# Optimization experiments

Measured on AMD Instinct MI355X. Metric: run time of the kernel, lower is better.

## Reference

```python
import jax, jax.numpy as jnp
import numpy as np


def setup_inputs() -> dict:
    key = jax.random.key(0)
    k_x, k_q, k_k, k_v = jax.random.split(key, 4)
    B, S, F, U = 8, 2048, 1024, 256
    x = jax.random.normal(k_x, (B, S, F), dtype=jnp.float32)
    Wq = jax.random.normal(k_q, (F, U), dtype=jnp.float32) * 0.05
    Wk = jax.random.normal(k_k, (F, U), dtype=jnp.float32) * 0.05
    Wv = jax.random.normal(k_v, (F, U), dtype=jnp.float32) * 0.05
    return {"x": x, "Wq": Wq, "Wk": Wk, "Wv": Wv}


def reference(x, Wq, Wk, Wv):
    # x: [B, S, F]; projections tanh-activated: [B, S, U]
    xQ = jnp.tanh(jnp.einsum("bsf,fu->bsu", x, Wq))
    xK = jnp.tanh(jnp.einsum("bsf,fu->bsu", x, Wk))
    xV = jnp.tanh(jnp.einsum("bsf,fu->bsu", x, Wv))
    scale = 1.0 / jnp.sqrt(jnp.asarray(x.shape[-1], dtype=jnp.float32))
    scores = jnp.einsum("bsu,btu->bst", xQ, xK) * scale  # [B, S, S]
    weights = jax.nn.softmax(scores, axis=-1)
    out = jnp.einsum("bst,btu->bsu", weights, xV)  # return_sequences=True
    return out
```

## Files before the change

kernel.cpp:

```cpp
#include <hip/hip_runtime.h>
#include <math.h>

#define B_ 8
#define S_ 2048
#define F_ 1024
#define U_ 256
#define M_ (B_ * S_)

typedef __attribute__((ext_vector_type(8))) short bf16x8;
typedef __attribute__((ext_vector_type(4))) float f32x4;
typedef __attribute__((ext_vector_type(16))) float f32x16;
typedef unsigned short ushort_t;

__device__ __forceinline__ unsigned short f2bf(float x) {
    unsigned u = __builtin_bit_cast(unsigned, x);
    unsigned r = (u + 0x7fffu + ((u >> 16) & 1u)) >> 16;
    return (unsigned short)r;
}
__device__ __forceinline__ float bf2f(unsigned short b) {
    return __builtin_bit_cast(float, ((unsigned)b) << 16);
}
__device__ __forceinline__ void gload16(const void* g, void* l) {
    __builtin_amdgcn_global_load_lds(
        (const __attribute__((address_space(1))) unsigned int*)g,
        (__attribute__((address_space(3))) unsigned int*)l, 16, 0, 0);
}
__device__ __forceinline__ f32x4 zero4() {
    f32x4 v; v[0] = 0.f; v[1] = 0.f; v[2] = 0.f; v[3] = 0.f; return v;
}

__global__ __launch_bounds__(256) void convw_kernel(
    const float* __restrict__ Wq, const float* __restrict__ Wk,
    const float* __restrict__ Wv, ushort_t* __restrict__ Wp)
{
    const int ks   = blockIdx.x;
    const int wsel = blockIdx.y;
    const float* __restrict__ W = (wsel == 0) ? Wq : (wsel == 1) ? Wk : Wv;
    const int n = threadIdx.x;

    bf16x8 hv, lv;
    #pragma unroll
    for (int j = 0; j < 8; ++j) {
        float v = W[(size_t)(ks * 8 + j) * U_ + n];
        ushort_t h = f2bf(v);
        hv[j] = (short)h;
        lv[j] = (short)f2bf(v - bf2f(h));
    }
    size_t base = (size_t)wsel * 524288;
    *reinterpret_cast<bf16x8*>(&Wp[base + ((size_t)ks) * 2048 + n * 8]) = hv;
    *reinterpret_cast<bf16x8*>(&Wp[base + ((size_t)(128 + ks)) * 2048 + n * 8]) = lv;
}

__global__ __launch_bounds__(256, 2) void proj_mfma_kernel(
    const float* __restrict__ x,
    const ushort_t* __restrict__ Wp,
    ushort_t* __restrict__ qh_g, ushort_t* __restrict__ kh_g,
    ushort_t* __restrict__ vth_g)
{
    __shared__ float    As[2][128 * 16];
    __shared__ ushort_t Bs[2][2 * 2 * 256 * 8];

    const int orig = blockIdx.x;
    const int xcd  = orig & 7;
    const int idx  = orig >> 3;
    const int q3   = idx / 3;
    const int wsel = idx - q3 * 3;
    const int rt   = xcd * 16 + q3;
    const int row0 = rt * 128;

    const int tid = threadIdx.x;
    const int l = tid & 63, w = tid >> 6;
    const int m = l & 31, hi = l >> 5;

    const ushort_t* __restrict__ WpB = Wp + (size_t)wsel * 524288;

    f32x16 acc[4][2];
    #pragma unroll
    for (int mr = 0; mr < 4; ++mr)
        #pragma unroll
        for (int nf = 0; nf < 2; ++nf)
            #pragma unroll
            for (int r = 0; r < 16; ++r) acc[mr][nf][r] = 0.f;

    auto stageA = [&](int buf, int ks) {
        #pragma unroll
        for (int i = 0; i < 2; ++i) {
            int c = i * 256 + tid;
            int r = c >> 2, cc = c & 3;
            int cs = cc ^ ((r + (r >> 2)) & 3);
            const float* src = x + (size_t)(row0 + r) * F_ + ks * 16 + cs * 4;
            gload16(src, (char*)&As[buf][0] + (size_t)(i * 256 + w * 64) * 16);
        }
    };
    auto stageB = [&](int buf, int ks) {
        #pragma unroll
        for (int i = 0; i < 4; ++i) {
            int c = i * 256 + tid;
            int half = c >> 9, rem = c & 511;
            size_t so = (size_t)half * 262144 + (size_t)ks * 4096 + rem * 8;
            gload16(WpB + so, (char*)&Bs[buf][0] + (size_t)(i * 256 + w * 64) * 16);
        }
    };

    stageA(0, 0);
    stageB(0, 0);
    __syncthreads();

    for (int ks = 0; ks < 64; ++ks) {
        const int cur = ks & 1;
        if (ks < 63) { stageA(cur ^ 1, ks + 1); stageB(cur ^ 1, ks + 1); }

        const float*    Ac = &As[cur][0];
        const ushort_t* Bc = &Bs[cur][0];

        bf16x8 ah[4];
        #pragma unroll
        for (int mr = 0; mr < 4; ++mr) {
            const int r   = mr * 32 + m;
            const int swz = (r + (r >> 2)) & 3;
            const float4 a0 = *reinterpret_cast<const float4*>(
                &Ac[(size_t)(r * 4 + ((2 * hi) ^ swz)) * 4]);
            const float4 a1 = *reinterpret_cast<const float4*>(
                &Ac[(size_t)(r * 4 + ((2 * hi + 1) ^ swz)) * 4]);
            const float af[8] = {a0.x, a0.y, a0.z, a0.w, a1.x, a1.y, a1.z, a1.w};
            #pragma unroll
            for (int j = 0; j < 8; ++j) ah[mr][j] = (short)f2bf(af[j]);
        }
        #pragma unroll
        for (int nf = 0; nf < 2; ++nf) {
            const int nn = w * 64 + nf * 32 + m;
            const bf16x8 bh = *reinterpret_cast<const bf16x8*>(
                &Bc[(size_t)(hi * 2048 + nn * 8)]);
            const bf16x8 bl = *reinterpret_cast<const bf16x8*>(
                &Bc[(size_t)(4096 + hi * 2048 + nn * 8)]);
            #pragma unroll
            for (int mr = 0; mr < 4; ++mr) {
                acc[mr][nf] = __builtin_amdgcn_mfma_f32_32x32x16_bf16(ah[mr], bh, acc[mr][nf], 0, 0, 0);
                acc[mr][nf] = __builtin_amdgcn_mfma_f32_32x32x16_bf16(ah[mr], bl, acc[mr][nf], 0, 0, 0);
            }
        }
        __syncthreads();
    }

    #pragma unroll
    for (int mr = 0; mr < 4; ++mr) {
        const int row_base = row0 + mr * 32;
        if (wsel < 2) {
            ushort_t* __restrict__ hp = (wsel == 0) ? qh_g : kh_g;
            #pragma unroll
            for (int nf = 0; nf < 2; ++nf) {
                const int u = w * 64 + nf * 32 + m;
                #pragma unroll
                for (int reg = 0; reg < 16; ++reg) {
                    const int rl = (reg & 3) + 8 * (reg >> 2) + 4 * hi;
                    hp[(size_t)(row_base + rl) * U_ + u] =
                        f2bf(tanhf(acc[mr][nf][reg]));
                }
            }
        } else {
            const int b     = row0 >> 11;
            const int s_blk = (row0 & 2047) + mr * 32;
            #pragma unroll
            for (int nf = 0; nf < 2; ++nf) {
                const int u = w * 64 + nf * 32 + m;
                #pragma unroll
                for (int rg = 0; rg < 4; ++rg) {
                    ushort4 hv;
                    hv.x = f2bf(tanhf(acc[mr][nf][rg * 4 + 0]));
                    hv.y = f2bf(tanhf(acc[mr][nf][rg * 4 + 1]));
                    hv.z = f2bf(tanhf(acc[mr][nf][rg * 4 + 2]));
                    hv.w = f2bf(tanhf(acc[mr][nf][rg * 4 + 3]));
                    size_t off = ((size_t)b * U_ + u) * S_ + s_blk + 8 * rg + 4 * hi;
                    *reinterpret_cast<ushort4*>(&vth_g[off]) = hv;
                }
            }
        }
    }
}

__global__ __launch_bounds__(256, 2) void attn_mfma_kernel(
    const ushort_t* __restrict__ qh_g,
    const ushort_t* __restrict__ kh_g,
    const ushort_t* __restrict__ vth_g,
    float* __restrict__ O0, float* __restrict__ O1,
    float* __restrict__ ml)
{
    __shared__ ushort_t Kbuf[2][32 * 256];
    __shared__ ushort_t Vbuf[2][256 * 40];
    __shared__ ushort_t Pbuf[4][512];

    const int tid = threadIdx.x;
    const int l  = tid & 63, w = tid >> 6;
    const int kq = l & 15,  g = l >> 4;

    const int logical = (blockIdx.x & 7) * 64 + (blockIdx.x >> 3);
    const int b     = logical >> 6;
    const int qb    = (logical >> 1) & 31;
    const int khalf = logical & 1;
    const int qrow0 = b * S_ + qb * 64 + w * 16;
    const int kb0   = khalf * 1024;

    bf16x8 qh[8];
    {
        const ushort_t* qbh = qh_g + (size_t)(qrow0 + kq) * U_;
        #pragma unroll
        for (int us = 0; us < 8; ++us)
            qh[us] = *reinterpret_cast<const bf16x8*>(qbh + us * 32 + g * 8);
    }

    f32x4 O[16];
    #pragma unroll
    for (int nt = 0; nt < 16; ++nt) O[nt] = zero4();
    float m_run = -INFINITY, l_run = 0.f;

    auto stage = [&](int buf, int k0) {
        #pragma unroll
        for (int i = 0; i < 4; ++i) {
            int c = w * 256 + i * 64 + l;
            int key = c >> 5, uc = c & 31;
            int ucs = uc ^ (key & 7);
            size_t so = (size_t)(b * S_ + k0 + key) * U_ + ucs * 8;
            gload16(kh_g + so, &Kbuf[buf][(w * 256 + i * 64) * 8]);
        }
        #pragma unroll
        for (int i = 0; i < 5; ++i) {
            int c = w * 320 + i * 64 + l;
            int u = (c * 52429) >> 18;
            int kc = c - u * 5;
            size_t so = ((size_t)b * U_ + u) * S_ + k0 + kc * 8;
            const ushort_t* sh = (kc < 4) ? (vth_g + so) : vth_g;
            gload16(sh, &Vbuf[buf][(w * 320 + i * 64) * 8]);
        }
    };

    stage(0, kb0);
    asm volatile("s_waitcnt vmcnt(0)" ::: "memory");
    __builtin_amdgcn_s_barrier();

    const float scale = 0.03125f;

    for (int t = 0; t < 32; ++t) {
        const int cur = t & 1;
        if (t < 31) stage(cur ^ 1, kb0 + (t + 1) * 32);

        const ushort_t* Kh = Kbuf[cur];
        const ushort_t* Vh = Vbuf[cur];

        f32x4 hh0 = zero4(), hh1 = zero4();
        #pragma unroll
        for (int us = 0; us < 8; ++us) {
            int off0 = kq * 256 + ((us * 32 + g * 8) ^ ((kq & 7) * 8));
            bf16x8 k0h = *reinterpret_cast<const bf16x8*>(Kh + off0);
            hh0 = __builtin_amdgcn_mfma_f32_16x16x32_bf16(k0h, qh[us], hh0, 0, 0, 0);
            int off1 = off0 + 16 * 256;
            bf16x8 k1h = *reinterpret_cast<const bf16x8*>(Kh + off1);
            hh1 = __builtin_amdgcn_mfma_f32_16x16x32_bf16(k1h, qh[us], hh1, 0, 0, 0);
        }
        f32x4 s0 = hh0 * scale;
        f32x4 s1 = hh1 * scale;

        float tm = fmaxf(fmaxf(fmaxf(s0[0], s0[1]), fmaxf(s0[2], s0[3])),
                         fmaxf(fmaxf(s1[0], s1[1]), fmaxf(s1[2], s1[3])));
        tm = fmaxf(tm, __shfl_xor(tm, 16));
        tm = fmaxf(tm, __shfl_xor(tm, 32));
        float mn = fmaxf(m_run, tm);
        ushort_t ph0[4], ph1[4];
        float su = 0.f;
        #pragma unroll
        for (int r = 0; r < 4; ++r) {
            ph0[r] = f2bf(expf(s0[r] - mn)); su += bf2f(ph0[r]);
        }
        #pragma unroll
        for (int r = 0; r < 4; ++r) {
            ph1[r] = f2bf(expf(s1[r] - mn)); su += bf2f(ph1[r]);
        }
        su += __shfl_xor(su, 16);
        su += __shfl_xor(su, 32);
        float f = expf(m_run - mn);
        l_run = l_run * f + su;
        m_run = mn;

        {
            ushort4 a, c;
            a.x = ph0[0]; a.y = ph0[1]; a.z = ph0[2]; a.w = ph0[3];
            c.x = ph1[0]; c.y = ph1[1]; c.z = ph1[2]; c.w = ph1[3];
            int pw0 = ((g >> 1)) * 128 + kq * 8 + (g & 1) * 4;
            int pw1 = (2 + (g >> 1)) * 128 + kq * 8 + (g & 1) * 4;
            *reinterpret_cast<ushort4*>(&Pbuf[w][pw0]) = a;
            *reinterpret_cast<ushort4*>(&Pbuf[w][pw1]) = c;
        }

        float fr0 = __shfl(f, g * 4 + 0), fr1 = __shfl(f, g * 4 + 1);
        float fr2 = __shfl(f, g * 4 + 2), fr3 = __shfl(f, g * 4 + 3);
        #pragma unroll
        for (int nt = 0; nt < 16; ++nt) {
            O[nt][0] *= fr0; O[nt][1] *= fr1; O[nt][2] *= fr2; O[nt][3] *= fr3;
        }

        bf16x8 pa_h = *reinterpret_cast<const bf16x8*>(&Pbuf[w][g * 128 + kq * 8]);
        #pragma unroll
        for (int nt = 0; nt < 16; ++nt) {
            int vo = (nt * 16 + kq) * 40 + g * 8;
            bf16x8 vh = *reinterpret_cast<const bf16x8*>(Vh + vo);
            O[nt] = __builtin_amdgcn_mfma_f32_16x16x32_bf16(pa_h, vh, O[nt], 0, 0, 0);
        }

        asm volatile("s_waitcnt vmcnt(0)" ::: "memory");
        __builtin_amdgcn_s_barrier();
    }

    float* __restrict__ Op = khalf ? O1 : O0;
    #pragma unroll
    for (int nt = 0; nt < 16; ++nt) {
        const int col = nt * 16 + kq;
        Op[(size_t)(qrow0 + g * 4 + 0) * U_ + col] = O[nt][0];
        Op[(size_t)(qrow0 + g * 4 + 1) * U_ + col] = O[nt][1];
        Op[(size_t)(qrow0 + g * 4 + 2) * U_ + col] = O[nt][2];
        Op[(size_t)(qrow0 + g * 4 + 3) * U_ + col] = O[nt][3];
    }
    if (g == 0) {
        ml[((size_t)khalf * M_ + qrow0 + kq) * 2 + 0] = m_run;
        ml[((size_t)khalf * M_ + qrow0 + kq) * 2 + 1] = l_run;
    }
}

__global__ __launch_bounds__(256) void merge_kernel(
    const float* __restrict__ O1, const float* __restrict__ ml,
    float* __restrict__ out)
{
    const int tid = threadIdx.x;
    const int row = blockIdx.x * 4 + (tid >> 6);
    const int c   = (tid & 63) * 4;

    const float m0 = ml[(size_t)row * 2 + 0];
    const float l0 = ml[(size_t)row * 2 + 1];
    const float m1 = ml[((size_t)M_ + row) * 2 + 0];
    const float l1 = ml[((size_t)M_ + row) * 2 + 1];
    const float Mx = fmaxf(m0, m1);
    float a0 = expf(m0 - Mx), a1 = expf(m1 - Mx);
    const float inv = 1.f / (a0 * l0 + a1 * l1);
    a0 *= inv; a1 *= inv;

    const size_t off = (size_t)row * U_ + c;
    const float4 o0 = *reinterpret_cast<const float4*>(out + off);
    const float4 o1 = *reinterpret_cast<const float4*>(O1 + off);
    float4 r;
    r.x = o0.x * a0 + o1.x * a1;
    r.y = o0.y * a0 + o1.y * a1;
    r.z = o0.z * a0 + o1.z * a1;
    r.w = o0.w * a0 + o1.w * a1;
    *reinterpret_cast<float4*>(out + off) = r;
}

extern "C" void kernel_launch(void* const* d_in, const int* in_sizes, int n_in,
                              void* d_out, int out_size, void* d_ws, size_t ws_size,
                              hipStream_t stream)
{
    (void)in_sizes; (void)n_in; (void)out_size; (void)ws_size;
    const float* x  = (const float*)d_in[0];
    const float* Wq = (const float*)d_in[1];
    const float* Wk = (const float*)d_in[2];
    const float* Wv = (const float*)d_in[3];
    float* out = (float*)d_out;

    ushort_t* ws = (ushort_t*)d_ws;
    const size_t T = (size_t)M_ * U_;
    ushort_t* qh_g  = ws;
    ushort_t* kh_g  = ws + T;
    ushort_t* vth_g = ws + 2 * T;
    ushort_t* Wp    = ws + 3 * T;
    float*    O1    = (float*)(ws + 3 * T + 1572864);
    float*    ml    = O1 + T;

    convw_kernel<<<dim3(128, 3), 256, 0, stream>>>(Wq, Wk, Wv, Wp);

    proj_mfma_kernel<<<dim3(384), 256, 0, stream>>>(
        x, Wp, qh_g, kh_g, vth_g);

    attn_mfma_kernel<<<dim3(512), 256, 0, stream>>>(
        qh_g, kh_g, vth_g, out, O1, ml);

    merge_kernel<<<dim3(M_ / 4), 256, 0, stream>>>(O1, ml, out);
}
```

Baseline: 181.8 us.

## Pre-convert x to bf16 and stage bf16 tiles in projection GEMM

Adds a pass that converts x to bf16 once into workspace. The projection kernel then loads bf16 tiles directly, with no per-iteration fp32-to-bf16 conversion in the inner loop. This halves the bytes each of the three weight-select blocks reads for x. The K step doubles to 32, so there are half as many iterations and barriers, and the LDS layout is simplified. The cost is an extra kernel launch plus a write and read of a 32MB bf16 copy. That copy aliases the O1 region, which relies on the workspace being large enough.

```diff
diff --git a/kernel.cpp b/kernel.cpp
--- a/kernel.cpp
+++ b/kernel.cpp
@@ -29,6 +29,23 @@
     f32x4 v; v[0] = 0.f; v[1] = 0.f; v[2] = 0.f; v[3] = 0.f; return v;
 }
 
+__global__ __launch_bounds__(256) void convx_kernel(
+    const float* __restrict__ x, ushort_t* __restrict__ xb)
+{
+    const size_t base = ((size_t)blockIdx.x * 256 + threadIdx.x) * 16;
+    #pragma unroll
+    for (int i = 0; i < 2; ++i) {
+        const float4 v0 = *reinterpret_cast<const float4*>(x + base + i * 8);
+        const float4 v1 = *reinterpret_cast<const float4*>(x + base + i * 8 + 4);
+        bf16x8 o;
+        o[0] = (short)f2bf(v0.x); o[1] = (short)f2bf(v0.y);
+        o[2] = (short)f2bf(v0.z); o[3] = (short)f2bf(v0.w);
+        o[4] = (short)f2bf(v1.x); o[5] = (short)f2bf(v1.y);
+        o[6] = (short)f2bf(v1.z); o[7] = (short)f2bf(v1.w);
+        *reinterpret_cast<bf16x8*>(xb + base + i * 8) = o;
+    }
+}
+
 __global__ __launch_bounds__(256) void convw_kernel(
     const float* __restrict__ Wq, const float* __restrict__ Wk,
     const float* __restrict__ Wv, ushort_t* __restrict__ Wp)
@@ -52,21 +69,20 @@
 }
 
 __global__ __launch_bounds__(256, 2) void proj_mfma_kernel(
-    const float* __restrict__ x,
+    const ushort_t* __restrict__ xb,
     const ushort_t* __restrict__ Wp,
     ushort_t* __restrict__ qh_g, ushort_t* __restrict__ kh_g,
     ushort_t* __restrict__ vth_g)
 {
-    __shared__ float    As[2][128 * 16];
-    __shared__ ushort_t Bs[2][2 * 2 * 256 * 8];
+    __shared__ ushort_t As[2][4 * 128 * 8];
+    __shared__ ushort_t Bs[2][2 * 4 * 256 * 8];
 
     const int orig = blockIdx.x;
     const int xcd  = orig & 7;
     const int idx  = orig >> 3;
     const int q3   = idx / 3;
     const int wsel = idx - q3 * 3;
-    const int rt   = xcd * 16 + q3;
-    const int row0 = rt * 128;
+    const int row0 = (xcd * 16 + q3) * 128;
 
     const int tid = threadIdx.x;
     const int l = tid & 63, w = tid >> 6;
@@ -85,20 +101,20 @@
     auto stageA = [&](int buf, int ks) {
         #pragma unroll
         for (int i = 0; i < 2; ++i) {
-            int c = i * 256 + tid;
-            int r = c >> 2, cc = c & 3;
-            int cs = cc ^ ((r + (r >> 2)) & 3);
-            const float* src = x + (size_t)(row0 + r) * F_ + ks * 16 + cs * 4;
+            int ci = i * 256 + tid;
+            int c = ci >> 7, r = ci & 127;
+            const ushort_t* src = xb + (size_t)(row0 + r) * F_ + ks * 32 + c * 8;
             gload16(src, (char*)&As[buf][0] + (size_t)(i * 256 + w * 64) * 16);
         }
     };
     auto stageB = [&](int buf, int ks) {
         #pragma unroll
-        for (int i = 0; i < 4; ++i) {
-            int c = i * 256 + tid;
-            int half = c >> 9, rem = c & 511;
-            size_t so = (size_t)half * 262144 + (size_t)ks * 4096 + rem * 8;
-            gload16(WpB + so, (char*)&Bs[buf][0] + (size_t)(i * 256 + w * 64) * 16);
+        for (int i = 0; i < 8; ++i) {
+            int ci = i * 256 + tid;
+            int half = ci >> 10, rem = ci & 1023;
+            const ushort_t* src = WpB + (size_t)half * 262144
+                                  + (size_t)ks * 8192 + rem * 8;
+            gload16(src, (char*)&Bs[buf][0] + (size_t)(i * 256 + w * 64) * 16);
         }
     };
 
@@ -106,37 +122,33 @@
     stageB(0, 0);
     __syncthreads();
 
-    for (int ks = 0; ks < 64; ++ks) {
+    for (int ks = 0; ks < 32; ++ks) {
         const int cur = ks & 1;
-        if (ks < 63) { stageA(cur ^ 1, ks + 1); stageB(cur ^ 1, ks + 1); }
-
-        const float*    Ac = &As[cur][0];
+        if (ks < 31) { stageA(cur ^ 1, ks + 1); stageB(cur ^ 1, ks + 1); }
+
+        const ushort_t* Ac = &As[cur][0];
         const ushort_t* Bc = &Bs[cur][0];
 
-        bf16x8 ah[4];
-        #pragma unroll
-        for (int mr = 0; mr < 4; ++mr) {
-            const int r   = mr * 32 + m;
-            const int swz = (r + (r >> 2)) & 3;
-            const float4 a0 = *reinterpret_cast<const float4*>(
-                &Ac[(size_t)(r * 4 + ((2 * hi) ^ swz)) * 4]);
-            const float4 a1 = *reinterpret_cast<const float4*>(
-                &Ac[(size_t)(r * 4 + ((2 * hi + 1) ^ swz)) * 4]);
-            const float af[8] = {a0.x, a0.y, a0.z, a0.w, a1.x, a1.y, a1.z, a1.w};
-            #pragma unroll
-            for (int j = 0; j < 8; ++j) ah[mr][j] = (short)f2bf(af[j]);
-        }
-        #pragma unroll
-        for (int nf = 0; nf < 2; ++nf) {
-            const int nn = w * 64 + nf * 32 + m;
-            const bf16x8 bh = *reinterpret_cast<const bf16x8*>(
-                &Bc[(size_t)(hi * 2048 + nn * 8)]);
-            const bf16x8 bl = *reinterpret_cast<const bf16x8*>(
-                &Bc[(size_t)(4096 + hi * 2048 + nn * 8)]);
-            #pragma unroll
-            for (int mr = 0; mr < 4; ++mr) {
-                acc[mr][nf] = __builtin_amdgcn_mfma_f32_32x32x16_bf16(ah[mr], bh, acc[mr][nf], 0, 0, 0);
-                acc[mr][nf] = __builtin_amdgcn_mfma_f32_32x32x16_bf16(ah[mr], bl, acc[mr][nf], 0, 0, 0);
+        #pragma unroll
+        for (int g = 0; g < 2; ++g) {
+            const int ksl = g * 2 + hi;
+            bf16x8 ah[4];
+            #pragma unroll
+            for (int mr = 0; mr < 4; ++mr)
+                ah[mr] = *reinterpret_cast<const bf16x8*>(
+                    &Ac[(size_t)(ksl * 128 + mr * 32 + m) * 8]);
+            #pragma unroll
+            for (int nf = 0; nf < 2; ++nf) {
+                const int nn = w * 64 + nf * 32 + m;
+                const bf16x8 bh = *reinterpret_cast<const bf16x8*>(
+                    &Bc[(size_t)(ksl * 2048 + nn * 8)]);
+                const bf16x8 bl = *reinterpret_cast<const bf16x8*>(
+                    &Bc[(size_t)(8192 + ksl * 2048 + nn * 8)]);
+                #pragma unroll
+                for (int mr = 0; mr < 4; ++mr) {
+                    acc[mr][nf] = __builtin_amdgcn_mfma_f32_32x32x16_bf16(ah[mr], bh, acc[mr][nf], 0, 0, 0);
+                    acc[mr][nf] = __builtin_amdgcn_mfma_f32_32x32x16_bf16(ah[mr], bl, acc[mr][nf], 0, 0, 0);
+                }
             }
         }
         __syncthreads();
@@ -369,13 +381,15 @@
     ushort_t* kh_g  = ws + T;
     ushort_t* vth_g = ws + 2 * T;
     ushort_t* Wp    = ws + 3 * T;
-    float*    O1    = (float*)(ws + 3 * T + 1572864);
+    ushort_t* xb    = ws + 3 * T + 1572864;
+    float*    O1    = (float*)xb;
     float*    ml    = O1 + T;
 
+    convx_kernel<<<dim3(4096), 256, 0, stream>>>(x, xb);
     convw_kernel<<<dim3(128, 3), 256, 0, stream>>>(Wq, Wk, Wv, Wp);
 
     proj_mfma_kernel<<<dim3(384), 256, 0, stream>>>(
-        x, Wp, qh_g, kh_g, vth_g);
+        xb, Wp, qh_g, kh_g, vth_g);
 
     attn_mfma_kernel<<<dim3(512), 256, 0, stream>>>(
         qh_g, kh_g, vth_g, out, O1, ml);
```

Result: no change. 179.0 us (-1.5%).

## Pre-convert x to bf16 transposed layout and deepen projection GEMM pipeline

Applied to the files above, without the earlier changes.

Adds a kernel that converts x to bf16 once, laid out in k-slab-major order. The projection GEMM, which reads each x tile three times (once per weight), now loads half as many bytes and skips the per-iteration fp32-to-bf16 conversion. The projection loop moves from double buffering to a 3-4 stage global-to-LDS pipeline with a partial vmcnt wait instead of a full __syncthreads. The attention loop's wait and barrier move to the top of each iteration. The cost is an extra pass over x plus a 32 MB write, and the xbt workspace is aliased with O1.

```diff
diff --git a/kernel.cpp b/kernel.cpp
--- a/kernel.cpp
+++ b/kernel.cpp
@@ -29,6 +29,36 @@
     f32x4 v; v[0] = 0.f; v[1] = 0.f; v[2] = 0.f; v[3] = 0.f; return v;
 }
 
+__global__ __launch_bounds__(256) void convxt_kernel(
+    const float* __restrict__ x, ushort_t* __restrict__ xbt)
+{
+    __shared__ ushort_t T[8][129][8];
+
+    const int t  = threadIdx.x;
+    const int r0 = blockIdx.x * 128;
+    const int k0 = blockIdx.y * 64;
+
+    #pragma unroll
+    for (int i = 0; i < 8; ++i) {
+        const int r = i * 16 + (t >> 4);
+        const int c = (t & 15) * 4;
+        const float4 v = *reinterpret_cast<const float4*>(
+            x + (size_t)(r0 + r) * F_ + k0 + c);
+        ushort4 o;
+        o.x = f2bf(v.x); o.y = f2bf(v.y); o.z = f2bf(v.z); o.w = f2bf(v.w);
+        *reinterpret_cast<ushort4*>(&T[c >> 3][r][c & 7]) = o;
+    }
+    __syncthreads();
+    #pragma unroll
+    for (int i = 0; i < 4; ++i) {
+        const int ci  = i * 256 + t;
+        const int ksl = ci >> 7, r = ci & 127;
+        ushort_t* dst = xbt + ((size_t)(blockIdx.y * 8 + ksl) * M_ + r0 + r) * 8;
+        *reinterpret_cast<bf16x8*>(dst) =
+            *reinterpret_cast<const bf16x8*>(&T[ksl][r][0]);
+    }
+}
+
 __global__ __launch_bounds__(256) void convw_kernel(
     const float* __restrict__ Wq, const float* __restrict__ Wk,
     const float* __restrict__ Wv, ushort_t* __restrict__ Wp)
@@ -52,21 +82,20 @@
 }
 
 __global__ __launch_bounds__(256, 2) void proj_mfma_kernel(
-    const float* __restrict__ x,
+    const ushort_t* __restrict__ xbt,
     const ushort_t* __restrict__ Wp,
     ushort_t* __restrict__ qh_g, ushort_t* __restrict__ kh_g,
     ushort_t* __restrict__ vth_g)
 {
-    __shared__ float    As[2][128 * 16];
-    __shared__ ushort_t Bs[2][2 * 2 * 256 * 8];
+    __shared__ ushort_t As[4][2 * 128 * 8];
+    __shared__ ushort_t Bs[3][2 * 2 * 256 * 8];
 
     const int orig = blockIdx.x;
     const int xcd  = orig & 7;
     const int idx  = orig >> 3;
     const int q3   = idx / 3;
     const int wsel = idx - q3 * 3;
-    const int rt   = xcd * 16 + q3;
-    const int row0 = rt * 128;
+    const int row0 = (xcd * 16 + q3) * 128;
 
     const int tid = threadIdx.x;
     const int l = tid & 63, w = tid >> 6;
@@ -83,63 +112,64 @@
             for (int r = 0; r < 16; ++r) acc[mr][nf][r] = 0.f;
 
     auto stageA = [&](int buf, int ks) {
-        #pragma unroll
-        for (int i = 0; i < 2; ++i) {
-            int c = i * 256 + tid;
-            int r = c >> 2, cc = c & 3;
-            int cs = cc ^ ((r + (r >> 2)) & 3);
-            const float* src = x + (size_t)(row0 + r) * F_ + ks * 16 + cs * 4;
-            gload16(src, (char*)&As[buf][0] + (size_t)(i * 256 + w * 64) * 16);
-        }
+        const int ksl = tid >> 7, r = tid & 127;
+        const ushort_t* src = xbt + ((size_t)(ks * 2 + ksl) * M_ + row0 + r) * 8;
+        gload16(src, (char*)&As[buf][0] + (size_t)(w * 64) * 16);
     };
     auto stageB = [&](int buf, int ks) {
         #pragma unroll
         for (int i = 0; i < 4; ++i) {
-            int c = i * 256 + tid;
-            int half = c >> 9, rem = c & 511;
-            size_t so = (size_t)half * 262144 + (size_t)ks * 4096 + rem * 8;
-            gload16(WpB + so, (char*)&Bs[buf][0] + (size_t)(i * 256 + w * 64) * 16);
+            const int ci = i * 256 + tid;
+            const int half = ci >> 9, rem = ci & 511;
+            const int ksl = rem >> 8, n = rem & 255;
+            const ushort_t* src = WpB + (size_t)half * 262144
+                                  + (size_t)(ks * 2 + ksl) * 2048 + n * 8;
+            gload16(src, (char*)&Bs[buf][0] + (size_t)(i * 256 + w * 64) * 16);
         }
     };
 
     stageA(0, 0);
     stageB(0, 0);
-    __syncthreads();
+    stageA(1, 1);
+    stageB(1, 1);
+    stageA(2, 2);
 
     for (int ks = 0; ks < 64; ++ks) {
-        const int cur = ks & 1;
-        if (ks < 63) { stageA(cur ^ 1, ks + 1); stageB(cur ^ 1, ks + 1); }
-
-        const float*    Ac = &As[cur][0];
-        const ushort_t* Bc = &Bs[cur][0];
+        if (ks < 62) asm volatile("s_waitcnt vmcnt(6)" ::: "memory");
+        else         asm volatile("s_waitcnt vmcnt(0)" ::: "memory");
+        __builtin_amdgcn_s_barrier();
+        if (ks + 2 < 64) stageB((ks + 2) % 3, ks + 2);
+        if (ks + 3 < 64) stageA((ks + 3) & 3, ks + 3);
+
+        const ushort_t* Ac = &As[ks & 3][0];
+        const ushort_t* Bc = &Bs[ks % 3][0];
 
         bf16x8 ah[4];
         #pragma unroll
-        for (int mr = 0; mr < 4; ++mr) {
-            const int r   = mr * 32 + m;
-            const int swz = (r + (r >> 2)) & 3;
-            const float4 a0 = *reinterpret_cast<const float4*>(
-                &Ac[(size_t)(r * 4 + ((2 * hi) ^ swz)) * 4]);
-            const float4 a1 = *reinterpret_cast<const float4*>(
-                &Ac[(size_t)(r * 4 + ((2 * hi + 1) ^ swz)) * 4]);
-            const float af[8] = {a0.x, a0.y, a0.z, a0.w, a1.x, a1.y, a1.z, a1.w};
-            #pragma unroll
-            for (int j = 0; j < 8; ++j) ah[mr][j] = (short)f2bf(af[j]);
-        }
+        for (int mr = 0; mr < 4; ++mr)
+            ah[mr] = *reinterpret_cast<const bf16x8*>(
+                &Ac[(size_t)(hi * 128 + mr * 32 + m) * 8]);
+        bf16x8 bh[2], bl[2];
         #pragma unroll
         for (int nf = 0; nf < 2; ++nf) {
             const int nn = w * 64 + nf * 32 + m;
-            const bf16x8 bh = *reinterpret_cast<const bf16x8*>(
-                &Bc[(size_t)(hi * 2048 + nn * 8)]);
-            const bf16x8 bl = *reinterpret_cast<const bf16x8*>(
-                &Bc[(size_t)(4096 + hi * 2048 + nn * 8)]);
+            bh[nf] = *reinterpret_cast<const bf16x8*>(
+                &Bc[(size_t)(hi * 256 + nn) * 8]);
+            bl[nf] = *reinterpret_cast<const bf16x8*>(
+                &Bc[(size_t)(512 + hi * 256 + nn) * 8]);
+        }
+        #pragma unroll
+        for (int nf = 0; nf < 2; ++nf)
             #pragma unroll
-            for (int mr = 0; mr < 4; ++mr) {
-                acc[mr][nf] = __builtin_amdgcn_mfma_f32_32x32x16_bf16(ah[mr], bh, acc[mr][nf], 0, 0, 0);
-                acc[mr][nf] = __builtin_amdgcn_mfma_f32_32x32x16_bf16(ah[mr], bl, acc[mr][nf], 0, 0, 0);
-            }
-        }
-        __syncthreads();
+            for (int mr = 0; mr < 4; ++mr)
+                acc[mr][nf] = __builtin_amdgcn_mfma_f32_32x32x16_bf16(
+                    ah[mr], bh[nf], acc[mr][nf], 0, 0, 0);
+        #pragma unroll
+        for (int nf = 0; nf < 2; ++nf)
+            #pragma unroll
+            for (int mr = 0; mr < 4; ++mr)
+                acc[mr][nf] = __builtin_amdgcn_mfma_f32_32x32x16_bf16(
+                    ah[mr], bl[nf], acc[mr][nf], 0, 0, 0);
     }
 
     #pragma unroll
@@ -234,13 +264,13 @@
     };
 
     stage(0, kb0);
-    asm volatile("s_waitcnt vmcnt(0)" ::: "memory");
-    __builtin_amdgcn_s_barrier();
 
     const float scale = 0.03125f;
 
     for (int t = 0; t < 32; ++t) {
         const int cur = t & 1;
+        asm volatile("s_waitcnt vmcnt(0)" ::: "memory");
+        __builtin_amdgcn_s_barrier();
         if (t < 31) stage(cur ^ 1, kb0 + (t + 1) * 32);
 
         const ushort_t* Kh = Kbuf[cur];
@@ -304,9 +334,6 @@
             bf16x8 vh = *reinterpret_cast<const bf16x8*>(Vh + vo);
             O[nt] = __builtin_amdgcn_mfma_f32_16x16x32_bf16(pa_h, vh, O[nt], 0, 0, 0);
         }
-
-        asm volatile("s_waitcnt vmcnt(0)" ::: "memory");
-        __builtin_amdgcn_s_barrier();
     }
 
     float* __restrict__ Op = khalf ? O1 : O0;
@@ -369,13 +396,15 @@
     ushort_t* kh_g  = ws + T;
     ushort_t* vth_g = ws + 2 * T;
     ushort_t* Wp    = ws + 3 * T;
-    float*    O1    = (float*)(ws + 3 * T + 1572864);
+    ushort_t* xbt   = ws + 3 * T + 1572864;
+    float*    O1    = (float*)xbt;
     float*    ml    = O1 + T;
 
+    convxt_kernel<<<dim3(128, 16), 256, 0, stream>>>(x, xbt);
     convw_kernel<<<dim3(128, 3), 256, 0, stream>>>(Wq, Wk, Wv, Wp);
 
     proj_mfma_kernel<<<dim3(384), 256, 0, stream>>>(
-        x, Wp, qh_g, kh_g, vth_g);
+        xbt, Wp, qh_g, kh_g, vth_g);
 
     attn_mfma_kernel<<<dim3(512), 256, 0, stream>>>(
         qh_g, kh_g, vth_g, out, O1, ml);
```

Result: no change. 179.4 us (-1.3%).
